# Kernel optimization log

Hardware: AMD Instinct MI355X
Metric: run time of the kernel (lower is better)

Reference implementation:

```python
import jax, jax.numpy as jnp
import numpy as np

N = 300000        # active voxels
C = 64            # channels (in_dim == out_dim)
K = 27            # 3x3x3 kernel offsets
EPS = 1e-5        # BatchNorm eps
GX, GY, GZ = 256, 256, 32  # voxel grid


def _build_neighbors():
    """Submanifold rulebook: for each active voxel, index of the active voxel at
    each of the 27 offsets, or -1 if that neighbor voxel is inactive."""
    rng = np.random.default_rng(0)
    lin = np.sort(rng.choice(GX * GY * GZ, size=N, replace=False))
    x, y, z = lin // (GY * GZ), (lin // GZ) % GY, lin % GZ
    nbr = np.full((N, K), -1, dtype=np.int32)
    k = 0
    for dx in (-1, 0, 1):
        for dy in (-1, 0, 1):
            for dz in (-1, 0, 1):
                nx, ny, nz = x + dx, y + dy, z + dz
                inb = (nx >= 0) & (nx < GX) & (ny >= 0) & (ny < GY) & (nz >= 0) & (nz < GZ)
                nl = (nx * GY + ny) * GZ + nz
                pos = np.searchsorted(lin, nl)
                posc = np.clip(pos, 0, N - 1)
                found = inb & (lin[posc] == nl)
                nbr[:, k] = np.where(found, posc, -1)
                k += 1
    return jnp.asarray(nbr)


def setup_inputs() -> dict:
    key = jax.random.key(0)
    k0, k1, k2 = jax.random.split(key, 3)
    return {
        "feats": jax.random.normal(k0, (N, C), dtype=jnp.float32),
        "W1": jax.random.normal(k1, (K, C, C), dtype=jnp.float32) * 0.05,
        "gamma1": jnp.ones((C,), jnp.float32),
        "beta1": jnp.zeros((C,), jnp.float32),
        "W2": jax.random.normal(k2, (K, C, C), dtype=jnp.float32) * 0.05,
        "gamma2": jnp.ones((C,), jnp.float32),
        "beta2": jnp.zeros((C,), jnp.float32),
        "neighbor_idx": _build_neighbors(),
    }


def _subm_conv(feats, W, nbr):
    # gather -> matmul -> accumulate, one pass per kernel offset (fixed K=27)
    mask = nbr >= 0
    idx = jnp.where(mask, nbr, 0)
    out = jnp.zeros((feats.shape[0], W.shape[-1]), feats.dtype)
    for k in range(K):
        g = feats[idx[:, k]] * mask[:, k:k + 1].astype(feats.dtype)  # [N, C]
        out = out + g @ W[k]
    return out


def _bn_relu(x, gamma, beta):
    # BatchNorm1d training-mode forward: biased batch stats over active voxels
    mu = jnp.mean(x, axis=0)
    var = jnp.var(x, axis=0)
    return jax.nn.relu((x - mu) * jax.lax.rsqrt(var + EPS) * gamma + beta)


def reference(feats, W1, gamma1, beta1, W2, gamma2, beta2, neighbor_idx):
    x_net = _bn_relu(_subm_conv(feats, W1, neighbor_idx), gamma1, beta1)
    res = _bn_relu(_subm_conv(x_net, W2, neighbor_idx), gamma2, beta2)
    return x_net + res
```

## Files before the change

kernel.cpp:

```cpp
#include <hip/hip_runtime.h>
#include <cstdint>
#include <cstddef>

typedef unsigned short u16;
typedef __bf16 bf16x8 __attribute__((ext_vector_type(8)));
typedef float f32x4 __attribute__((ext_vector_type(4)));

#define KOFF 27
#define EPSBN 1e-5f

__device__ inline u16 f2bf(float f) {
  unsigned int u = __float_as_uint(f);
  unsigned int r = (u + 0x7FFFu + ((u >> 16) & 1u)) >> 16;
  return (u16)r;
}
__device__ inline float bf2f(u16 h) {
  return __uint_as_float(((unsigned int)h) << 16);
}

__global__ void k_prep(const float* __restrict__ feats, const float* __restrict__ W1,
                       const float* __restrict__ W2, const int* __restrict__ nbr,
                       u16* __restrict__ featsb, u16* __restrict__ w1p,
                       u16* __restrict__ w2p, int* __restrict__ nbrT,
                       float* __restrict__ stats, int N, int gN, int gW, int n4) {
  __shared__ int L[64 * KOFF];
  const int t = threadIdx.x;
  const int bid = blockIdx.x;

  if (bid < gN) {
    const int v0 = bid * 64;
    const int nv = min(64, N - v0);
    const int cnt = nv * KOFF;
    for (int i = t; i < cnt; i += 256) L[i] = nbr[(size_t)v0 * KOFF + i];
    __syncthreads();
    for (int i = t; i < KOFF * 64; i += 256) {
      int k = i >> 6, j = i & 63;
      if (j < nv) nbrT[(size_t)k * N + v0 + j] = L[j * KOFF + k];
    }
    return;
  }
  if (bid < gN + 2 * gW) {
    const int wi = bid - gN;
    const bool second = wi >= gW;
    const float* W = second ? W2 : W1;
    u16* Wp = second ? w2p : w1p;
    const int tid = (second ? wi - gW : wi) * 256 + t;
    if (tid >= KOFF * 4096) return;
    const int k = tid >> 12;
    const int rem = tid & 4095;
    const int slot = rem >> 3;
    const int e = rem & 7;
    const int ks = slot >> 8;
    const int ct = (slot >> 6) & 3;
    const int lane = slot & 63;
    const int j = ks * 32 + ((lane >> 4) << 3) + e;
    const int c = ct * 16 + (lane & 15);
    Wp[tid] = f2bf(W[(k * 64 + j) * 64 + c]);
    return;
  }
  const int idx = bid - gN - 2 * gW;
  if (idx == 0) stats[t] = 0.f;
  const int i = idx * 256 + t;
  if (i >= n4) return;
  const float4 v = reinterpret_cast<const float4*>(feats)[i];
  ushort4 o;
  o.x = f2bf(v.x); o.y = f2bf(v.y); o.z = f2bf(v.z); o.w = f2bf(v.w);
  reinterpret_cast<ushort4*>(featsb)[i] = o;
}

__launch_bounds__(256, 3)
__global__ void k_conv(const u16* __restrict__ F, const u16* __restrict__ Wp,
                       const int* __restrict__ nbrT, float* __restrict__ out,
                       float* __restrict__ stats, int N) {
  const int t = threadIdx.x;
  const int w = t >> 6;
  const int lane = t & 63;
  const int vbase = blockIdx.x * 256 + (w << 6) + (lane & 15);
  const int ch = (lane >> 4) << 3;

  f32x4 acc[4][4];
#pragma unroll
  for (int m = 0; m < 4; ++m)
#pragma unroll
    for (int c = 0; c < 4; ++c) acc[m][c] = (f32x4){0.f, 0.f, 0.f, 0.f};

  int nid[4];
#pragma unroll
  for (int m = 0; m < 4; ++m) {
    const int v = vbase + (m << 4);
    nid[m] = (v < N) ? nbrT[v] : -1;
  }

  const u16* bp = Wp + ((size_t)lane << 3);

#pragma unroll 3
  for (int k = 0; k < KOFF; ++k) {
    bf16x8 bfr[2][4];
#pragma unroll
    for (int ks = 0; ks < 2; ++ks)
#pragma unroll
      for (int c = 0; c < 4; ++c)
        bfr[ks][c] = *reinterpret_cast<const bf16x8*>(bp + ((size_t)k << 12) + (ks << 11) + (c << 9));

    bf16x8 a0[4], a1[4];
#pragma unroll
    for (int m = 0; m < 4; ++m) {
      a0[m] = (bf16x8){};
      a1[m] = (bf16x8){};
      const int id = nid[m];
      if (id >= 0) {
        const u16* fr = F + ((size_t)id << 6) + ch;
        a0[m] = *reinterpret_cast<const bf16x8*>(fr);
        a1[m] = *reinterpret_cast<const bf16x8*>(fr + 32);
      }
    }

    if (k + 1 < KOFF) {
      const int* nk = nbrT + (size_t)(k + 1) * N;
#pragma unroll
      for (int m = 0; m < 4; ++m) {
        const int v = vbase + (m << 4);
        nid[m] = (v < N) ? nk[v] : -1;
      }
    }

#pragma unroll
    for (int m = 0; m < 4; ++m)
#pragma unroll
      for (int c = 0; c < 4; ++c)
        acc[m][c] = __builtin_amdgcn_mfma_f32_16x16x32_bf16(a0[m], bfr[0][c], acc[m][c], 0, 0, 0);
#pragma unroll
    for (int m = 0; m < 4; ++m)
#pragma unroll
      for (int c = 0; c < 4; ++c)
        acc[m][c] = __builtin_amdgcn_mfma_f32_16x16x32_bf16(a1[m], bfr[1][c], acc[m][c], 0, 0, 0);
  }

  const int row0 = blockIdx.x * 256 + (w << 6) + ((lane >> 4) << 2);
#pragma unroll
  for (int m = 0; m < 4; ++m) {
#pragma unroll
    for (int c = 0; c < 4; ++c) {
      const int col = (c << 4) + (lane & 15);
#pragma unroll
      for (int e = 0; e < 4; ++e) {
        const int v = row0 + (m << 4) + e;
        if (v < N) out[((size_t)v << 6) + col] = acc[m][c][e];
      }
    }
  }

  __shared__ float sred[4][128];
#pragma unroll
  for (int c = 0; c < 4; ++c) {
    float s = 0.f, q = 0.f;
#pragma unroll
    for (int m = 0; m < 4; ++m)
#pragma unroll
      for (int e = 0; e < 4; ++e) {
        const float x = acc[m][c][e];
        s += x;
        q += x * x;
      }
    s += __shfl_xor(s, 16, 64);
    s += __shfl_xor(s, 32, 64);
    q += __shfl_xor(q, 16, 64);
    q += __shfl_xor(q, 32, 64);
    if (lane < 16) {
      sred[w][(c << 4) + lane] = s;
      sred[w][64 + (c << 4) + lane] = q;
    }
  }
  __syncthreads();
  if (t < 128) {
    const float tot = sred[0][t] + sred[1][t] + sred[2][t] + sred[3][t];
    atomicAdd(&stats[t], tot);
  }
}


__global__ void k_final(const float* __restrict__ stats, const float* __restrict__ gamma,
                        const float* __restrict__ beta, float* __restrict__ sb, int N) {
  const int c = threadIdx.x;
  const float inv = 1.0f / (float)N;
  const float mu = stats[c] * inv;
  const float var = stats[64 + c] * inv - mu * mu;
  const float sc = gamma[c] * rsqrtf(var + EPSBN);
  sb[c] = sc;
  sb[64 + c] = beta[c] - mu * sc;
}

__global__ void k_apply1(const float* __restrict__ x, const float* __restrict__ sb,
                         u16* __restrict__ xb, int n4) {
  int i = blockIdx.x * 256 + threadIdx.x;
  if (i >= n4) return;
  const int cg = i & 15;
  float4 v = reinterpret_cast<const float4*>(x)[i];
  const float4 sc = reinterpret_cast<const float4*>(sb)[cg];
  const float4 bi = reinterpret_cast<const float4*>(sb)[16 + cg];
  float y0 = fmaxf(0.f, v.x * sc.x + bi.x);
  float y1 = fmaxf(0.f, v.y * sc.y + bi.y);
  float y2 = fmaxf(0.f, v.z * sc.z + bi.z);
  float y3 = fmaxf(0.f, v.w * sc.w + bi.w);
  ushort4 o;
  o.x = f2bf(y0); o.y = f2bf(y1); o.z = f2bf(y2); o.w = f2bf(y3);
  reinterpret_cast<ushort4*>(xb)[i] = o;
}

__global__ void k_apply2(float* __restrict__ io, const float* __restrict__ sb,
                         const u16* __restrict__ xb, int n4) {
  int i = blockIdx.x * 256 + threadIdx.x;
  if (i >= n4) return;
  const int cg = i & 15;
  float4 v = reinterpret_cast<const float4*>(io)[i];
  const float4 sc = reinterpret_cast<const float4*>(sb)[cg];
  const float4 bi = reinterpret_cast<const float4*>(sb)[16 + cg];
  const ushort4 xn = reinterpret_cast<const ushort4*>(xb)[i];
  float4 o;
  o.x = bf2f(xn.x) + fmaxf(0.f, v.x * sc.x + bi.x);
  o.y = bf2f(xn.y) + fmaxf(0.f, v.y * sc.y + bi.y);
  o.z = bf2f(xn.z) + fmaxf(0.f, v.z * sc.z + bi.z);
  o.w = bf2f(xn.w) + fmaxf(0.f, v.w * sc.w + bi.w);
  reinterpret_cast<float4*>(io)[i] = o;
}


extern "C" void kernel_launch(void* const* d_in, const int* in_sizes, int n_in,
                              void* d_out, int out_size, void* d_ws, size_t ws_size,
                              hipStream_t stream) {
  const float* feats = (const float*)d_in[0];
  const float* W1 = (const float*)d_in[1];
  const float* g1 = (const float*)d_in[2];
  const float* b1 = (const float*)d_in[3];
  const float* W2 = (const float*)d_in[4];
  const float* g2 = (const float*)d_in[5];
  const float* b2 = (const float*)d_in[6];
  const int* nbr = (const int*)d_in[7];
  const int N = in_sizes[0] / 64;

  char* ws = (char*)d_ws;
  size_t off = 0;
  auto alloc = [&](size_t bytes) {
    void* p = ws + off;
    off = (off + bytes + 255) & ~(size_t)255;
    return p;
  };
  u16* featsb = (u16*)alloc((size_t)N * 64 * 2);
  u16* xnetb = (u16*)alloc((size_t)N * 64 * 2);
  u16* w1p = (u16*)alloc((size_t)KOFF * 4096 * 2);
  u16* w2p = (u16*)alloc((size_t)KOFF * 4096 * 2);
  float* stats = (float*)alloc(256 * 4);
  float* sb1 = (float*)alloc(128 * 4);
  float* sb2 = (float*)alloc(128 * 4);
  int* nbrT = (int*)alloc((size_t)KOFF * N * 4);
  float* outf = (float*)d_out;

  const int n4 = N * 16;
  const int gN = (N + 63) / 64;
  const int gPrep = (n4 + 255) / 256;
  const int gW = (KOFF * 4096 + 255) / 256;
  const int gConv = (N + 255) / 256;

  k_prep<<<gN + 2 * gW + gPrep, 256, 0, stream>>>(feats, W1, W2, nbr, featsb, w1p, w2p,
                                                  nbrT, stats, N, gN, gW, n4);

  k_conv<<<gConv, 256, 0, stream>>>(featsb, w1p, nbrT, outf, stats, N);
  k_final<<<1, 64, 0, stream>>>(stats, g1, b1, sb1, N);
  k_apply1<<<gPrep, 256, 0, stream>>>(outf, sb1, xnetb, n4);

  k_conv<<<gConv, 256, 0, stream>>>(xnetb, w2p, nbrT, outf, stats + 128, N);
  k_final<<<1, 64, 0, stream>>>(stats + 128, g2, b2, sb2, N);
  k_apply2<<<gPrep, 256, 0, stream>>>(outf, sb2, xnetb, n4);
}
```

Before: 259.0 us.

## Double-buffer neighbor feature gathers into LDS via async global_load_lds

The conv kernel now gathers neighbor feature rows with asynchronous global-to-LDS loads into a per-wave double buffer with an XOR swizzle. The rows for offset k+1 load while the MFMAs for offset k run, and neighbor indices are fetched two offsets ahead. Missing neighbors point at a zero buffer instead of taking a branch. This aims to hide gather latency behind compute, at the cost of 64KB of LDS per block and lower occupancy (launch bounds drop from 3 to 2), plus a hand-written vmcnt wait that must match the number of loads in flight.

```diff
diff --git a/kernel.cpp b/kernel.cpp
--- a/kernel.cpp
+++ b/kernel.cpp
@@ -18,11 +18,18 @@
   return __uint_as_float(((unsigned int)h) << 16);
 }
 
+typedef const __attribute__((address_space(1))) void ga_void;
+typedef __attribute__((address_space(3))) void lds_void;
+__device__ __forceinline__ void gload_lds16(const void* g, void* l) {
+  __builtin_amdgcn_global_load_lds((ga_void*)g, (lds_void*)l, 16, 0, 0);
+}
+
 __global__ void k_prep(const float* __restrict__ feats, const float* __restrict__ W1,
                        const float* __restrict__ W2, const int* __restrict__ nbr,
                        u16* __restrict__ featsb, u16* __restrict__ w1p,
                        u16* __restrict__ w2p, int* __restrict__ nbrT,
-                       float* __restrict__ stats, int N, int gN, int gW, int n4) {
+                       float* __restrict__ stats, float* __restrict__ zbuf,
+                       int N, int gN, int gW, int n4) {
   __shared__ int L[64 * KOFF];
   const int t = threadIdx.x;
   const int bid = blockIdx.x;
@@ -37,6 +44,7 @@
       int k = i >> 6, j = i & 63;
       if (j < nv) nbrT[(size_t)k * N + v0 + j] = L[j * KOFF + k];
     }
+    if (t < nv) nbrT[(size_t)KOFF * N + v0 + t] = -1;
     return;
   }
   if (bid < gN + 2 * gW) {
@@ -59,7 +67,10 @@
     return;
   }
   const int idx = bid - gN - 2 * gW;
-  if (idx == 0) stats[t] = 0.f;
+  if (idx == 0) {
+    stats[t] = 0.f;
+    if (t < 32) zbuf[t] = 0.f;
+  }
   const int i = idx * 256 + t;
   if (i >= n4) return;
   const float4 v = reinterpret_cast<const float4*>(feats)[i];
@@ -68,15 +79,23 @@
   reinterpret_cast<ushort4*>(featsb)[i] = o;
 }
 
-__launch_bounds__(256, 3)
+__launch_bounds__(256, 2)
 __global__ void k_conv(const u16* __restrict__ F, const u16* __restrict__ Wp,
-                       const int* __restrict__ nbrT, float* __restrict__ out,
-                       float* __restrict__ stats, int N) {
+                       const int* __restrict__ nbrT, const u16* __restrict__ zbuf,
+                       float* __restrict__ out, float* __restrict__ stats, int N) {
+  __shared__ u16 Ab[4][2][4096];
+  __shared__ float sred[4][128];
   const int t = threadIdx.x;
   const int w = t >> 6;
   const int lane = t & 63;
-  const int vbase = blockIdx.x * 256 + (w << 6) + (lane & 15);
-  const int ch = (lane >> 4) << 3;
+  const int v0w = blockIdx.x * 256 + (w << 6);
+  const int lr = lane >> 3;
+  const int swzch = ((lane & 7) ^ lr) << 3;
+  const u16* zsrc = zbuf + swzch;
+
+  const int r_lo = (lane & 15) << 6;
+  const int p0 = (((lane >> 4) ^ (lane & 7)) << 3);
+  const int p1 = (((4 ^ (lane >> 4)) ^ (lane & 7)) << 3);
 
   f32x4 acc[4][4];
 #pragma unroll
@@ -84,46 +103,68 @@
 #pragma unroll
     for (int c = 0; c < 4; ++c) acc[m][c] = (f32x4){0.f, 0.f, 0.f, 0.f};
 
-  int nid[4];
-#pragma unroll
-  for (int m = 0; m < 4; ++m) {
-    const int v = vbase + (m << 4);
-    nid[m] = (v < N) ? nbrT[v] : -1;
-  }
-
+  u16* const buf0 = &Ab[w][0][0];
+  u16* const buf1 = &Ab[w][1][0];
   const u16* bp = Wp + ((size_t)lane << 3);
 
-#pragma unroll 3
-  for (int k = 0; k < KOFF; ++k) {
+  int idc[8], idn[8];
+
+  {
+    const int* np = nbrT;
+#pragma unroll
+    for (int i = 0; i < 8; ++i) {
+      const int v = v0w + (i << 3) + lr;
+      const int id_ = np[min(v, N - 1)];
+      idc[i] = (v < N) ? id_ : -1;
+    }
+#pragma unroll
+    for (int i = 0; i < 8; ++i) {
+      const int id_ = idc[i];
+      const u16* s = (id_ >= 0) ? F + ((size_t)(unsigned)id_ << 6) + swzch : zsrc;
+      gload_lds16(s, buf0 + (i << 9));
+    }
+    const int* np1 = nbrT + (size_t)N;
+#pragma unroll
+    for (int i = 0; i < 8; ++i) {
+      const int v = v0w + (i << 3) + lr;
+      const int id_ = np1[min(v, N - 1)];
+      idc[i] = (v < N) ? id_ : -1;
+    }
+  }
+
+  auto conv_step = [&](int k, const u16* bufcur, u16* bufnxt,
+                       int(&ids_st)[8], int(&ids_ld)[8]) __attribute__((always_inline)) {
     bf16x8 bfr[2][4];
-#pragma unroll
-    for (int ks = 0; ks < 2; ++ks)
-#pragma unroll
-      for (int c = 0; c < 4; ++c)
-        bfr[ks][c] = *reinterpret_cast<const bf16x8*>(bp + ((size_t)k << 12) + (ks << 11) + (c << 9));
-
+    {
+      const u16* bk = bp + ((size_t)k << 12);
+#pragma unroll
+      for (int ks = 0; ks < 2; ++ks)
+#pragma unroll
+        for (int c = 0; c < 4; ++c)
+          bfr[ks][c] = *reinterpret_cast<const bf16x8*>(bk + (ks << 11) + (c << 9));
+    }
+    {
+      const int* np = nbrT + (size_t)(k + 2) * N;
+#pragma unroll
+      for (int i = 0; i < 8; ++i) {
+        const int v = v0w + (i << 3) + lr;
+        const int id_ = np[min(v, N - 1)];
+        ids_ld[i] = (v < N) ? id_ : -1;
+      }
+    }
+#pragma unroll
+    for (int i = 0; i < 8; ++i) {
+      const int id_ = ids_st[i];
+      const u16* s = (id_ >= 0) ? F + ((size_t)(unsigned)id_ << 6) + swzch : zsrc;
+      gload_lds16(s, bufnxt + (i << 9));
+    }
+    asm volatile("s_waitcnt vmcnt(24)" ::: "memory");
     bf16x8 a0[4], a1[4];
 #pragma unroll
     for (int m = 0; m < 4; ++m) {
-      a0[m] = (bf16x8){};
-      a1[m] = (bf16x8){};
-      const int id = nid[m];
-      if (id >= 0) {
-        const u16* fr = F + ((size_t)id << 6) + ch;
-        a0[m] = *reinterpret_cast<const bf16x8*>(fr);
-        a1[m] = *reinterpret_cast<const bf16x8*>(fr + 32);
-      }
-    }
-
-    if (k + 1 < KOFF) {
-      const int* nk = nbrT + (size_t)(k + 1) * N;
-#pragma unroll
-      for (int m = 0; m < 4; ++m) {
-        const int v = vbase + (m << 4);
-        nid[m] = (v < N) ? nk[v] : -1;
-      }
-    }
-
+      a0[m] = *reinterpret_cast<const bf16x8*>(bufcur + (m << 10) + r_lo + p0);
+      a1[m] = *reinterpret_cast<const bf16x8*>(bufcur + (m << 10) + r_lo + p1);
+    }
 #pragma unroll
     for (int m = 0; m < 4; ++m)
 #pragma unroll
@@ -134,9 +175,15 @@
 #pragma unroll
       for (int c = 0; c < 4; ++c)
         acc[m][c] = __builtin_amdgcn_mfma_f32_16x16x32_bf16(a1[m], bfr[1][c], acc[m][c], 0, 0, 0);
-  }
-
-  const int row0 = blockIdx.x * 256 + (w << 6) + ((lane >> 4) << 2);
+  };
+
+  for (int k = 0; k < 26; k += 2) {
+    conv_step(k, buf0, buf1, idc, idn);
+    conv_step(k + 1, buf1, buf0, idn, idc);
+  }
+  conv_step(26, buf0, buf1, idc, idn);
+
+  const int row0 = v0w + ((lane >> 4) << 2);
 #pragma unroll
   for (int m = 0; m < 4; ++m) {
 #pragma unroll
@@ -150,7 +197,6 @@
     }
   }
 
-  __shared__ float sred[4][128];
 #pragma unroll
   for (int c = 0; c < 4; ++c) {
     float s = 0.f, q = 0.f;
@@ -252,7 +298,8 @@
   float* stats = (float*)alloc(256 * 4);
   float* sb1 = (float*)alloc(128 * 4);
   float* sb2 = (float*)alloc(128 * 4);
-  int* nbrT = (int*)alloc((size_t)KOFF * N * 4);
+  float* zbuf = (float*)alloc(128);
+  int* nbrT = (int*)alloc((size_t)(KOFF + 2) * N * 4);
   float* outf = (float*)d_out;
 
   const int n4 = N * 16;
@@ -262,13 +309,13 @@
   const int gConv = (N + 255) / 256;
 
   k_prep<<<gN + 2 * gW + gPrep, 256, 0, stream>>>(feats, W1, W2, nbr, featsb, w1p, w2p,
-                                                  nbrT, stats, N, gN, gW, n4);
-
-  k_conv<<<gConv, 256, 0, stream>>>(featsb, w1p, nbrT, outf, stats, N);
+                                                  nbrT, stats, zbuf, N, gN, gW, n4);
+
+  k_conv<<<gConv, 256, 0, stream>>>(featsb, w1p, nbrT, (const u16*)zbuf, outf, stats, N);
   k_final<<<1, 64, 0, stream>>>(stats, g1, b1, sb1, N);
   k_apply1<<<gPrep, 256, 0, stream>>>(outf, sb1, xnetb, n4);
 
-  k_conv<<<gConv, 256, 0, stream>>>(xnetb, w2p, nbrT, outf, stats + 128, N);
+  k_conv<<<gConv, 256, 0, stream>>>(xnetb, w2p, nbrT, (const u16*)zbuf, outf, stats + 128, N);
   k_final<<<1, 64, 0, stream>>>(stats + 128, g2, b2, sb2, N);
   k_apply2<<<gPrep, 256, 0, stream>>>(outf, sb2, xnetb, n4);
 }
```

After: 290.0 us. 12.0% more time.
